# Kernel tuning notes

Measured on AMD Instinct MI355X. Metric: run time of the kernel, lower is better.

Reference implementation:

```python
import jax, jax.numpy as jnp
import numpy as np
from jax import lax

P_COARSE, P_FINE = 8, 4
EMBED_DIM = 128


def _patchify(x, p):
    # torch unfold(kernel=p, stride=p) then transpose: [B, Hp*Wp, C*p*p]
    B, C, H, W = x.shape
    Hp, Wp = H // p, W // p
    t = x.reshape(B, C, Hp, p, Wp, p).transpose(0, 2, 4, 1, 3, 5)
    return t.reshape(B, Hp * Wp, C * p * p), Hp, Wp


def _edge_map(x):
    gray = x.mean(axis=1, keepdims=True)
    kx = jnp.array([[-1., 0., 1.], [-2., 0., 2.], [-1., 0., 1.]], gray.dtype)[None, None]
    ky = jnp.array([[-1., -2., -1.], [0., 0., 0.], [1., 2., 1.]], gray.dtype)[None, None]
    pad = [(1, 1), (1, 1)]
    sx = lax.conv_general_dilated(gray, kx, (1, 1), pad)
    sy = lax.conv_general_dilated(gray, ky, (1, 1), pad)
    e = jnp.sqrt(sx * sx + sy * sy)
    B, _, H, W = e.shape
    # avg_pool2d(4, stride=4)
    return e.reshape(B, 1, H // 4, 4, W // 4, 4).mean(axis=(3, 5))


def _compact(tok, m):
    # stream-compact masked rows to the front, zero-pad the rest (pad_sequence semantics, padded to full Nf)
    Nf, D = tok.shape
    pos = jnp.cumsum(m) - 1
    pos = jnp.where(m, pos, Nf)  # unmasked rows go to overflow slot
    out = jnp.zeros((Nf + 1, D), tok.dtype).at[pos].set(tok)
    return out[:Nf]


def setup_inputs() -> dict:
    key = jax.random.key(0)
    ks = jax.random.split(key, 6)
    D = EMBED_DIM
    pd_c = 1 * P_COARSE * P_COARSE
    pd_f = 1 * P_FINE * P_FINE
    return {
        "x": jax.random.normal(ks[0], (8, 1, 512, 512), jnp.float32),
        "w_coarse": jax.random.normal(ks[1], (pd_c, D), jnp.float32) / np.sqrt(pd_c),
        "b_coarse": jnp.zeros((D,), jnp.float32),
        "w_fine": jax.random.normal(ks[2], (pd_f, D), jnp.float32) / np.sqrt(pd_f),
        "b_fine": jnp.zeros((D,), jnp.float32),
        "type_emb": jax.random.normal(ks[3], (2, D), jnp.float32) * 0.02,
    }


def reference(x, w_coarse, b_coarse, w_fine, b_fine, type_emb):
    B = x.shape[0]
    # coarse branch
    pc, Hc, Wc = _patchify(x, P_COARSE)
    coarse = pc @ w_coarse + b_coarse + type_emb[0]  # [B, Nc, D]
    # edge-driven mask
    edges = _edge_map(x)  # [B,1,He,We]
    mask = edges > edges.mean(axis=(2, 3), keepdims=True)
    # fine branch
    pf, Hf, Wf = _patchify(x, P_FINE)
    fine = pf @ w_fine + b_fine  # [B, Nf, D]
    # nearest upsample mask to (Hf, Wf): integer factor repeat
    m = mask[:, 0]
    m = jnp.repeat(jnp.repeat(m, Hf // m.shape[1], axis=1), Wf // m.shape[2], axis=2)
    mask_flat = m.reshape(B, -1)  # [B, Nf]
    fine_c = jax.vmap(_compact)(fine, mask_flat) + type_emb[1]
    tokens = jnp.concatenate([coarse, fine_c], axis=1)
    return tokens, mask_flat
```

## Files before the change

kernel.cpp:

```cpp
#include <hip/hip_runtime.h>

#define IMH 512
#define IMW 512
#define BATCH 8
#define NTOK 20480
#define NC 4096
#define NF 16384
#define ED 128

typedef float vf4 __attribute__((ext_vector_type(4)));

__device__ __forceinline__ void nt_store4(float* p, float a, float b, float c, float d) {
    vf4 v = {a, b, c, d};
    __builtin_nontemporal_store(v, (vf4*)p);
}
__device__ __forceinline__ void nt_store4v(float* p, float4 v) {
    nt_store4(p, v.x, v.y, v.z, v.w);
}

__global__ __launch_bounds__(256) void fused_edge_coarse(const float* __restrict__ x,
                                                         const float* __restrict__ wc,
                                                         const float* __restrict__ bc,
                                                         const float* __restrict__ temb,
                                                         float* __restrict__ out,
                                                         double* __restrict__ edges) {
    __shared__ float esm[66][68];
    int blk = blockIdx.x;
    int t = threadIdx.x;
    if (blk < 1024) {
        int b = blk >> 7;
        int pblk = (blk & 127) * 32;
        int wv = __builtin_amdgcn_readfirstlane(t >> 6);
        int lane = t & 63;
        int h = wv & 1;
        int p0 = pblk + (wv >> 1) * 16;
        int d = h * 64 + lane;
        float wcol[64];
        #pragma unroll
        for (int k = 0; k < 64; ++k) wcol[k] = wc[k * ED + d];
        float base = bc[d] + temb[d];
        const float* img = x + ((size_t)b * IMH + (p0 >> 6) * 8) * IMW + (p0 & 63) * 8;
        float* dst = out + ((size_t)b * NTOK + p0) * ED + d;
        #pragma unroll
        for (int p = 0; p < 16; ++p) {
            const float* pimg = img + p * 8;
            float acc = base;
            #pragma unroll
            for (int r = 0; r < 8; ++r) {
                const float* rp = pimg + r * IMW;
                acc += rp[0] * wcol[r * 8 + 0] + rp[1] * wcol[r * 8 + 1]
                     + rp[2] * wcol[r * 8 + 2] + rp[3] * wcol[r * 8 + 3]
                     + rp[4] * wcol[r * 8 + 4] + rp[5] * wcol[r * 8 + 5]
                     + rp[6] * wcol[r * 8 + 6] + rp[7] * wcol[r * 8 + 7];
            }
            __builtin_nontemporal_store(acc, dst + (size_t)p * ED);
        }
    } else {
        int blk2 = blk - 1024;
        int b = blk2 >> 6;
        int tile = blk2 & 63;
        int ty0 = (tile >> 3) * 64;
        int tx0 = (tile & 7) * 64;
        const float* img = x + (size_t)b * (IMH * IMW);
        for (int idx = t; idx < 66 * 66; idx += 256) {
            int r = idx / 66, c = idx - r * 66;
            int gy = ty0 - 1 + r, gx = tx0 - 1 + c;
            float v = 0.f;
            if (gy >= 0 && gy < IMH && gx >= 0 && gx < IMW) v = img[gy * IMW + gx];
            esm[r][c] = v;
        }
        __syncthreads();
        int cy = t >> 4, cx = t & 15;
        double acc = 0.0;
        #pragma unroll
        for (int dy = 0; dy < 4; ++dy) {
            int py = cy * 4 + dy + 1;
            #pragma unroll
            for (int dx = 0; dx < 4; ++dx) {
                int px = cx * 4 + dx + 1;
                double a00 = (double)esm[py - 1][px - 1];
                double a01 = (double)esm[py - 1][px];
                double a02 = (double)esm[py - 1][px + 1];
                double a10 = (double)esm[py][px - 1];
                double a12 = (double)esm[py][px + 1];
                double a20 = (double)esm[py + 1][px - 1];
                double a21 = (double)esm[py + 1][px];
                double a22 = (double)esm[py + 1][px + 1];
                double sx = (a02 + 2.0 * a12 + a22) - (a00 + 2.0 * a10 + a20);
                double sy = (a20 + 2.0 * a21 + a22) - (a00 + 2.0 * a01 + a02);
                acc += sqrt(sx * sx + sy * sy);
            }
        }
        int gy = (ty0 >> 2) + cy;
        int gx = (tx0 >> 2) + cx;
        edges[((size_t)b << 14) + gy * 128 + gx] = acc * (1.0 / 16.0);
    }
}

__global__ __launch_bounds__(1024) void scan_kernel(const double* __restrict__ edges,
                                                    int* __restrict__ pos,
                                                    int* __restrict__ Karr,
                                                    float* __restrict__ mask_out) {
    int b = blockIdx.x;
    const double* e = edges + ((size_t)b << 14);
    int t = threadIdx.x;
    int lane = t & 63, wid = t >> 6;
    double v[16];
    #pragma unroll
    for (int j = 0; j < 8; ++j) {
        double2 dv = *(const double2*)&e[t * 16 + j * 2];
        v[2 * j] = dv.x; v[2 * j + 1] = dv.y;
    }
    double s = 0.0;
    #pragma unroll
    for (int j = 0; j < 16; ++j) s += v[j];
    #pragma unroll
    for (int off = 32; off > 0; off >>= 1) s += __shfl_xor(s, off);
    __shared__ double wsum[16];
    __shared__ int wcnt[16];
    if (lane == 0) wsum[wid] = s;
    __syncthreads();
    double total = 0.0;
    #pragma unroll
    for (int w = 0; w < 16; ++w) total += wsum[w];
    double mean = total * (1.0 / 16384.0);
    int m[16], cnt = 0;
    #pragma unroll
    for (int j = 0; j < 16; ++j) { m[j] = (v[j] > mean) ? 1 : 0; cnt += m[j]; }
    int incl = cnt;
    #pragma unroll
    for (int off = 1; off < 64; off <<= 1) {
        int up = __shfl_up(incl, off);
        if (lane >= off) incl += up;
    }
    if (lane == 63) wcnt[wid] = incl;
    __syncthreads();
    int woff = 0, Ktot = 0;
    #pragma unroll
    for (int w = 0; w < 16; ++w) { int c = wcnt[w]; Ktot += c; if (w < wid) woff += c; }
    int run = woff + incl - cnt;
    float mf[16]; int pv[16];
    #pragma unroll
    for (int j = 0; j < 16; ++j) {
        pv[j] = m[j] ? run : -1;
        run += m[j];
        mf[j] = m[j] ? 1.0f : 0.0f;
    }
    float* mb = mask_out + ((size_t)b << 14) + t * 16;
    int* pb = pos + ((size_t)b << 14) + t * 16;
    #pragma unroll
    for (int q = 0; q < 4; ++q) {
        nt_store4(&mb[q * 4], mf[4 * q], mf[4 * q + 1], mf[4 * q + 2], mf[4 * q + 3]);
        *(int4*)&pb[q * 4] = make_int4(pv[4 * q], pv[4 * q + 1], pv[4 * q + 2], pv[4 * q + 3]);
    }
    if (t == 0) Karr[b] = Ktot;
}

__global__ __launch_bounds__(256) void fine_kernel(const float* __restrict__ x,
                                                   const float* __restrict__ wfp,
                                                   const float* __restrict__ bfp,
                                                   const float* __restrict__ temb,
                                                   const int* __restrict__ pos,
                                                   const int* __restrict__ Karr,
                                                   float* __restrict__ out) {
    int b = blockIdx.y;
    int i0 = blockIdx.x * 64;
    int hf = i0 >> 7;
    int wf0 = i0 & 127;
    int t = threadIdx.x;
    int d4 = t & 31;
    int g = t >> 5;
    __shared__ float smx[4][256];
    float4 wcol[16];
    #pragma unroll
    for (int k = 0; k < 16; ++k) wcol[k] = *(const float4*)&wfp[k * ED + d4 * 4];
    const float* img = x + ((size_t)b * IMH + hf * 4) * IMW + wf0 * 4;
    {
        int r = t >> 6, c4 = t & 63;
        *(float4*)&smx[r][c4 * 4] = *(const float4*)&img[r * IMW + c4 * 4];
    }
    __syncthreads();
    int K = Karr[b];
    const int* posb = pos + ((size_t)b << 14);
    float4 fill = *(const float4*)&temb[ED + d4 * 4];
    float4 bse = *(const float4*)&bfp[d4 * 4];
    float4 base = make_float4(bse.x + fill.x, bse.y + fill.y, bse.z + fill.z, bse.w + fill.w);
    float* tok = out + ((size_t)b * NTOK + NC) * ED;
    #pragma unroll
    for (int pp = 0; pp < 8; ++pp) {
        int p = g + pp * 8;
        int i = i0 + p;
        int ps = posb[i];
        if (ps >= 0) {
            float4 acc = base;
            #pragma unroll
            for (int r = 0; r < 4; ++r) {
                float4 vv = *(const float4*)&smx[r][p * 4];
                acc.x += vv.x * wcol[4 * r].x + vv.y * wcol[4 * r + 1].x + vv.z * wcol[4 * r + 2].x + vv.w * wcol[4 * r + 3].x;
                acc.y += vv.x * wcol[4 * r].y + vv.y * wcol[4 * r + 1].y + vv.z * wcol[4 * r + 2].y + vv.w * wcol[4 * r + 3].y;
                acc.z += vv.x * wcol[4 * r].z + vv.y * wcol[4 * r + 1].z + vv.z * wcol[4 * r + 2].z + vv.w * wcol[4 * r + 3].z;
                acc.w += vv.x * wcol[4 * r].w + vv.y * wcol[4 * r + 1].w + vv.z * wcol[4 * r + 2].w + vv.w * wcol[4 * r + 3].w;
            }
            nt_store4v(tok + ((size_t)ps * 32 + d4) * 4, acc);
        }
        if (i >= K) {
            nt_store4v(tok + ((size_t)i * 32 + d4) * 4, fill);
        }
    }
}

extern "C" void kernel_launch(void* const* d_in, const int* in_sizes, int n_in,
                              void* d_out, int out_size, void* d_ws, size_t ws_size,
                              hipStream_t stream) {
    const float* x    = (const float*)d_in[0];
    const float* wc   = (const float*)d_in[1];
    const float* bc   = (const float*)d_in[2];
    const float* wfp  = (const float*)d_in[3];
    const float* bfp  = (const float*)d_in[4];
    const float* temb = (const float*)d_in[5];
    float* out = (float*)d_out;

    double* edges = (double*)d_ws;
    int* pos  = (int*)((char*)d_ws + (size_t)BATCH * NF * sizeof(double));
    int* Karr = (int*)((char*)d_ws + (size_t)BATCH * NF * (sizeof(double) + sizeof(int)));

    float* mask_out = out + (size_t)BATCH * NTOK * ED;

    fused_edge_coarse<<<dim3(1536), 256, 0, stream>>>(x, wc, bc, temb, out, edges);
    scan_kernel<<<dim3(BATCH), 1024, 0, stream>>>(edges, pos, Karr, mask_out);
    fine_kernel<<<dim3(256, BATCH), 256, 0, stream>>>(x, wfp, bfp, temb, pos, Karr, out);
}
```

Baseline: 49.23 us.

## Fold scan into fine kernel using per-tile edge partial sums and bitmasks

Removes the separate single-block-per-batch scan kernel. The edge kernel now writes per-tile partial sums, and each fine block recomputes the batch mean, the mask bits and the prefix counts for its row from the edges buffer. Compaction positions come from popcount over 64-bit masks instead of a stored pos array. This saves one launch and a serialized 8-block kernel, at the cost of every fine block redundantly reading 128KB of edges per batch.

After: 51.22 us. +4.0%, slower.

```diff
diff --git a/kernel.cpp b/kernel.cpp
--- a/kernel.cpp
+++ b/kernel.cpp
@@ -18,20 +18,22 @@
     nt_store4(p, v.x, v.y, v.z, v.w);
 }
 
-__global__ __launch_bounds__(256) void fused_edge_coarse(const float* __restrict__ x,
-                                                         const float* __restrict__ wc,
-                                                         const float* __restrict__ bc,
-                                                         const float* __restrict__ temb,
-                                                         float* __restrict__ out,
-                                                         double* __restrict__ edges) {
+__global__ __launch_bounds__(256) void k1_edge_coarse(const float* __restrict__ x,
+                                                      const float* __restrict__ wc,
+                                                      const float* __restrict__ bc,
+                                                      const float* __restrict__ temb,
+                                                      float* __restrict__ out,
+                                                      double* __restrict__ edges,
+                                                      double* __restrict__ tsum) {
     __shared__ float esm[66][68];
+    __shared__ double dred[4];
     int blk = blockIdx.x;
     int t = threadIdx.x;
+    int lane = t & 63, wid = t >> 6;
     if (blk < 1024) {
         int b = blk >> 7;
         int pblk = (blk & 127) * 32;
         int wv = __builtin_amdgcn_readfirstlane(t >> 6);
-        int lane = t & 63;
         int h = wv & 1;
         int p0 = pblk + (wv >> 1) * 16;
         int d = h * 64 + lane;
@@ -91,108 +93,105 @@
                 acc += sqrt(sx * sx + sy * sy);
             }
         }
+        double cell = acc * (1.0 / 16.0);
         int gy = (ty0 >> 2) + cy;
         int gx = (tx0 >> 2) + cx;
-        edges[((size_t)b << 14) + gy * 128 + gx] = acc * (1.0 / 16.0);
-    }
-}
-
-__global__ __launch_bounds__(1024) void scan_kernel(const double* __restrict__ edges,
-                                                    int* __restrict__ pos,
-                                                    int* __restrict__ Karr,
-                                                    float* __restrict__ mask_out) {
-    int b = blockIdx.x;
-    const double* e = edges + ((size_t)b << 14);
+        edges[((size_t)b << 14) + gy * 128 + gx] = cell;
+        double sc = cell;
+        #pragma unroll
+        for (int off = 32; off > 0; off >>= 1) sc += __shfl_xor(sc, off);
+        if (lane == 0) dred[wid] = sc;
+        __syncthreads();
+        if (t == 0) tsum[b * 64 + tile] = dred[0] + dred[1] + dred[2] + dred[3];
+    }
+}
+
+__global__ __launch_bounds__(256) void k2_fine(const float* __restrict__ x,
+                                               const float* __restrict__ wfp,
+                                               const float* __restrict__ bfp,
+                                               const float* __restrict__ temb,
+                                               const double* __restrict__ edges,
+                                               const double* __restrict__ tsum,
+                                               float* __restrict__ out,
+                                               float* __restrict__ mask_out) {
+    int b = blockIdx.y;
+    int row = blockIdx.x;
     int t = threadIdx.x;
     int lane = t & 63, wid = t >> 6;
-    double v[16];
-    #pragma unroll
-    for (int j = 0; j < 8; ++j) {
-        double2 dv = *(const double2*)&e[t * 16 + j * 2];
-        v[2 * j] = dv.x; v[2 * j + 1] = dv.y;
-    }
-    double s = 0.0;
-    #pragma unroll
-    for (int j = 0; j < 16; ++j) s += v[j];
-    #pragma unroll
-    for (int off = 32; off > 0; off >>= 1) s += __shfl_xor(s, off);
-    __shared__ double wsum[16];
-    __shared__ int wcnt[16];
-    if (lane == 0) wsum[wid] = s;
-    __syncthreads();
+    __shared__ float smx[4][512];
+    __shared__ int excl_s[256];
+    __shared__ unsigned long long bits_s[256];
+    __shared__ int wtot[4];
+
+    const double* ts = tsum + b * 64;
     double total = 0.0;
     #pragma unroll
-    for (int w = 0; w < 16; ++w) total += wsum[w];
+    for (int j = 0; j < 64; ++j) total += ts[j];
     double mean = total * (1.0 / 16384.0);
-    int m[16], cnt = 0;
-    #pragma unroll
-    for (int j = 0; j < 16; ++j) { m[j] = (v[j] > mean) ? 1 : 0; cnt += m[j]; }
+
+    const double* e = edges + ((size_t)b << 14) + t * 64;
+    unsigned long long mybits = 0ULL;
+    #pragma unroll
+    for (int j = 0; j < 32; ++j) {
+        double2 dv = *(const double2*)&e[j * 2];
+        if (dv.x > mean) mybits |= (1ULL << (2 * j));
+        if (dv.y > mean) mybits |= (1ULL << (2 * j + 1));
+    }
+    int cnt = __popcll(mybits);
     int incl = cnt;
     #pragma unroll
     for (int off = 1; off < 64; off <<= 1) {
         int up = __shfl_up(incl, off);
         if (lane >= off) incl += up;
     }
-    if (lane == 63) wcnt[wid] = incl;
+    if (lane == 63) wtot[wid] = incl;
+    bits_s[t] = mybits;
     __syncthreads();
-    int woff = 0, Ktot = 0;
-    #pragma unroll
-    for (int w = 0; w < 16; ++w) { int c = wcnt[w]; Ktot += c; if (w < wid) woff += c; }
-    int run = woff + incl - cnt;
-    float mf[16]; int pv[16];
-    #pragma unroll
-    for (int j = 0; j < 16; ++j) {
-        pv[j] = m[j] ? run : -1;
-        run += m[j];
-        mf[j] = m[j] ? 1.0f : 0.0f;
-    }
-    float* mb = mask_out + ((size_t)b << 14) + t * 16;
-    int* pb = pos + ((size_t)b << 14) + t * 16;
-    #pragma unroll
-    for (int q = 0; q < 4; ++q) {
-        nt_store4(&mb[q * 4], mf[4 * q], mf[4 * q + 1], mf[4 * q + 2], mf[4 * q + 3]);
-        *(int4*)&pb[q * 4] = make_int4(pv[4 * q], pv[4 * q + 1], pv[4 * q + 2], pv[4 * q + 3]);
-    }
-    if (t == 0) Karr[b] = Ktot;
-}
-
-__global__ __launch_bounds__(256) void fine_kernel(const float* __restrict__ x,
-                                                   const float* __restrict__ wfp,
-                                                   const float* __restrict__ bfp,
-                                                   const float* __restrict__ temb,
-                                                   const int* __restrict__ pos,
-                                                   const int* __restrict__ Karr,
-                                                   float* __restrict__ out) {
-    int b = blockIdx.y;
-    int i0 = blockIdx.x * 64;
-    int hf = i0 >> 7;
-    int wf0 = i0 & 127;
-    int t = threadIdx.x;
+    int woff = 0, K = 0;
+    #pragma unroll
+    for (int w = 0; w < 4; ++w) { int c = wtot[w]; K += c; if (w < wid) woff += c; }
+    excl_s[t] = woff + incl - cnt;
+
+    const float* img = x + ((size_t)b * IMH + row * 4) * IMW;
+    #pragma unroll
+    for (int k = 0; k < 2; ++k) {
+        int idx = t + 256 * k;
+        int r = idx >> 7, c4 = idx & 127;
+        *(float4*)&smx[r][c4 * 4] = *(const float4*)&img[r * IMW + c4 * 4];
+    }
+    __syncthreads();
+
+    int base = excl_s[2 * row];
+    unsigned long long lo = bits_s[2 * row];
+    unsigned long long hi = bits_s[2 * row + 1];
+
+    if (t < 128) {
+        unsigned long long bb = (t < 64) ? lo : hi;
+        float mv = ((bb >> (t & 63)) & 1ULL) ? 1.0f : 0.0f;
+        __builtin_nontemporal_store(mv, mask_out + ((size_t)b << 14) + row * 128 + t);
+    }
+
     int d4 = t & 31;
     int g = t >> 5;
-    __shared__ float smx[4][256];
     float4 wcol[16];
     #pragma unroll
     for (int k = 0; k < 16; ++k) wcol[k] = *(const float4*)&wfp[k * ED + d4 * 4];
-    const float* img = x + ((size_t)b * IMH + hf * 4) * IMW + wf0 * 4;
-    {
-        int r = t >> 6, c4 = t & 63;
-        *(float4*)&smx[r][c4 * 4] = *(const float4*)&img[r * IMW + c4 * 4];
-    }
-    __syncthreads();
-    int K = Karr[b];
-    const int* posb = pos + ((size_t)b << 14);
     float4 fill = *(const float4*)&temb[ED + d4 * 4];
     float4 bse = *(const float4*)&bfp[d4 * 4];
-    float4 base = make_float4(bse.x + fill.x, bse.y + fill.y, bse.z + fill.z, bse.w + fill.w);
+    float4 fbase = make_float4(bse.x + fill.x, bse.y + fill.y, bse.z + fill.z, bse.w + fill.w);
     float* tok = out + ((size_t)b * NTOK + NC) * ED;
-    #pragma unroll
-    for (int pp = 0; pp < 8; ++pp) {
+    int i0 = row * 128;
+    #pragma unroll
+    for (int pp = 0; pp < 16; ++pp) {
         int p = g + pp * 8;
         int i = i0 + p;
-        int ps = posb[i];
-        if (ps >= 0) {
-            float4 acc = base;
+        unsigned long long bb = (p < 64) ? lo : hi;
+        if ((bb >> (p & 63)) & 1ULL) {
+            int below = (p < 64)
+                ? __popcll(lo & ((1ULL << p) - 1))
+                : __popcll(lo) + __popcll(hi & ((1ULL << (p - 64)) - 1));
+            int ps = base + below;
+            float4 acc = fbase;
             #pragma unroll
             for (int r = 0; r < 4; ++r) {
                 float4 vv = *(const float4*)&smx[r][p * 4];
@@ -220,13 +219,11 @@
     const float* temb = (const float*)d_in[5];
     float* out = (float*)d_out;
 
-    double* edges = (double*)d_ws;
-    int* pos  = (int*)((char*)d_ws + (size_t)BATCH * NF * sizeof(double));
-    int* Karr = (int*)((char*)d_ws + (size_t)BATCH * NF * (sizeof(double) + sizeof(int)));
-
+    char* wsb = (char*)d_ws;
+    double* edges = (double*)wsb;
+    double* tsum  = (double*)(wsb + (size_t)BATCH * NF * 8);
     float* mask_out = out + (size_t)BATCH * NTOK * ED;
 
-    fused_edge_coarse<<<dim3(1536), 256, 0, stream>>>(x, wc, bc, temb, out, edges);
-    scan_kernel<<<dim3(BATCH), 1024, 0, stream>>>(edges, pos, Karr, mask_out);
-    fine_kernel<<<dim3(256, BATCH), 256, 0, stream>>>(x, wfp, bfp, temb, pos, Karr, out);
-}
+    k1_edge_coarse<<<dim3(1536), 256, 0, stream>>>(x, wc, bc, temb, out, edges, tsum);
+    k2_fine<<<dim3(128, BATCH), 256, 0, stream>>>(x, wfp, bfp, temb, edges, tsum, out, mask_out);
+}
```

## Move coarse projection into fine kernel and precompute per-tile edge sums

Applied to the files above, without the earlier changes.

Splits the edge computation into its own kernel, which also emits per-tile partial sums so the scan no longer reduces the whole edge map itself. The coarse patch projection moves out of the first kernel into a combined coarse+fine kernel, where each block handles two fine tiles. Nontemporal stores are replaced with normal stores. This shortens the critical path ahead of the scan and removes a launch's worth of tail, but leaves the coarse work waiting on the serial scan instead of overlapping with it.

Result: slower. 54.68 us (+11.1%).

```diff
diff --git a/kernel.cpp b/kernel.cpp
--- a/kernel.cpp
+++ b/kernel.cpp
@@ -8,30 +8,133 @@
 #define NF 16384
 #define ED 128
 
-typedef float vf4 __attribute__((ext_vector_type(4)));
-
-__device__ __forceinline__ void nt_store4(float* p, float a, float b, float c, float d) {
-    vf4 v = {a, b, c, d};
-    __builtin_nontemporal_store(v, (vf4*)p);
-}
-__device__ __forceinline__ void nt_store4v(float* p, float4 v) {
-    nt_store4(p, v.x, v.y, v.z, v.w);
-}
-
-__global__ __launch_bounds__(256) void fused_edge_coarse(const float* __restrict__ x,
-                                                         const float* __restrict__ wc,
-                                                         const float* __restrict__ bc,
-                                                         const float* __restrict__ temb,
-                                                         float* __restrict__ out,
-                                                         double* __restrict__ edges) {
+__global__ __launch_bounds__(256) void k_edge(const float* __restrict__ x,
+                                              double* __restrict__ edges,
+                                              double* __restrict__ tsum) {
     __shared__ float esm[66][68];
+    __shared__ double dred[4];
     int blk = blockIdx.x;
     int t = threadIdx.x;
-    if (blk < 1024) {
-        int b = blk >> 7;
-        int pblk = (blk & 127) * 32;
+    int lane = t & 63, wid = t >> 6;
+    int b = blk >> 6;
+    int tile = blk & 63;
+    int ty0 = (tile >> 3) * 64;
+    int tx0 = (tile & 7) * 64;
+    const float* img = x + (size_t)b * (IMH * IMW);
+    for (int idx = t; idx < 66 * 66; idx += 256) {
+        int r = idx / 66, c = idx - r * 66;
+        int gy = ty0 - 1 + r, gx = tx0 - 1 + c;
+        float v = 0.f;
+        if (gy >= 0 && gy < IMH && gx >= 0 && gx < IMW) v = img[gy * IMW + gx];
+        esm[r][c] = v;
+    }
+    __syncthreads();
+    int cy = t >> 4, cx = t & 15;
+    double acc = 0.0;
+    #pragma unroll
+    for (int dy = 0; dy < 4; ++dy) {
+        int py = cy * 4 + dy + 1;
+        #pragma unroll
+        for (int dx = 0; dx < 4; ++dx) {
+            int px = cx * 4 + dx + 1;
+            double a00 = (double)esm[py - 1][px - 1];
+            double a01 = (double)esm[py - 1][px];
+            double a02 = (double)esm[py - 1][px + 1];
+            double a10 = (double)esm[py][px - 1];
+            double a12 = (double)esm[py][px + 1];
+            double a20 = (double)esm[py + 1][px - 1];
+            double a21 = (double)esm[py + 1][px];
+            double a22 = (double)esm[py + 1][px + 1];
+            double sx = (a02 + 2.0 * a12 + a22) - (a00 + 2.0 * a10 + a20);
+            double sy = (a20 + 2.0 * a21 + a22) - (a00 + 2.0 * a01 + a02);
+            acc += sqrt(sx * sx + sy * sy);
+        }
+    }
+    double cell = acc * (1.0 / 16.0);
+    int gy = (ty0 >> 2) + cy;
+    int gx = (tx0 >> 2) + cx;
+    edges[((size_t)b << 14) + gy * 128 + gx] = cell;
+    double sc = cell;
+    #pragma unroll
+    for (int off = 32; off > 0; off >>= 1) sc += __shfl_xor(sc, off);
+    if (lane == 0) dred[wid] = sc;
+    __syncthreads();
+    if (t == 0) tsum[b * 64 + tile] = dred[0] + dred[1] + dred[2] + dred[3];
+}
+
+__global__ __launch_bounds__(1024) void k_scan(const double* __restrict__ edges,
+                                               const double* __restrict__ tsum,
+                                               int* __restrict__ pos,
+                                               int* __restrict__ Karr,
+                                               float* __restrict__ mask_out) {
+    int b = blockIdx.x;
+    int t = threadIdx.x;
+    int lane = t & 63, wid = t >> 6;
+    __shared__ int wcnt[16];
+    const double* ts = tsum + b * 64;
+    double total = 0.0;
+    #pragma unroll
+    for (int j = 0; j < 64; ++j) total += ts[j];
+    double mean = total * (1.0 / 16384.0);
+
+    const double* e = edges + ((size_t)b << 14);
+    double v[16];
+    #pragma unroll
+    for (int j = 0; j < 8; ++j) {
+        double2 dv = *(const double2*)&e[t * 16 + j * 2];
+        v[2 * j] = dv.x; v[2 * j + 1] = dv.y;
+    }
+    int m[16], cnt = 0;
+    #pragma unroll
+    for (int j = 0; j < 16; ++j) { m[j] = (v[j] > mean) ? 1 : 0; cnt += m[j]; }
+    int incl = cnt;
+    #pragma unroll
+    for (int off = 1; off < 64; off <<= 1) {
+        int up = __shfl_up(incl, off);
+        if (lane >= off) incl += up;
+    }
+    if (lane == 63) wcnt[wid] = incl;
+    __syncthreads();
+    int woff = 0, Ktot = 0;
+    #pragma unroll
+    for (int w = 0; w < 16; ++w) { int c = wcnt[w]; Ktot += c; if (w < wid) woff += c; }
+    int run = woff + incl - cnt;
+    float mf[16]; int pv[16];
+    #pragma unroll
+    for (int j = 0; j < 16; ++j) {
+        pv[j] = m[j] ? run : -1;
+        run += m[j];
+        mf[j] = m[j] ? 1.0f : 0.0f;
+    }
+    float* mb = mask_out + ((size_t)b << 14) + t * 16;
+    int* pb = pos + ((size_t)b << 14) + t * 16;
+    #pragma unroll
+    for (int q = 0; q < 4; ++q) {
+        *(float4*)&mb[q * 4] = make_float4(mf[4 * q], mf[4 * q + 1], mf[4 * q + 2], mf[4 * q + 3]);
+        *(int4*)&pb[q * 4] = make_int4(pv[4 * q], pv[4 * q + 1], pv[4 * q + 2], pv[4 * q + 3]);
+    }
+    if (t == 0) Karr[b] = Ktot;
+}
+
+__global__ __launch_bounds__(256) void k_mega(const float* __restrict__ x,
+                                              const float* __restrict__ wc,
+                                              const float* __restrict__ bc,
+                                              const float* __restrict__ wfp,
+                                              const float* __restrict__ bfp,
+                                              const float* __restrict__ temb,
+                                              const int* __restrict__ pos,
+                                              const int* __restrict__ Karr,
+                                              float* __restrict__ out) {
+    __shared__ float smx[4][256];
+    int blk = blockIdx.x;
+    int t = threadIdx.x;
+    int lane = t & 63;
+    int b = blk >> 7;
+    int r128 = blk & 127;
+
+    {
+        int pblk = r128 * 32;
         int wv = __builtin_amdgcn_readfirstlane(t >> 6);
-        int lane = t & 63;
         int h = wv & 1;
         int p0 = pblk + (wv >> 1) * 16;
         int d = h * 64 + lane;
@@ -53,158 +156,55 @@
                      + rp[4] * wcol[r * 8 + 4] + rp[5] * wcol[r * 8 + 5]
                      + rp[6] * wcol[r * 8 + 6] + rp[7] * wcol[r * 8 + 7];
             }
-            __builtin_nontemporal_store(acc, dst + (size_t)p * ED);
-        }
-    } else {
-        int blk2 = blk - 1024;
-        int b = blk2 >> 6;
-        int tile = blk2 & 63;
-        int ty0 = (tile >> 3) * 64;
-        int tx0 = (tile & 7) * 64;
-        const float* img = x + (size_t)b * (IMH * IMW);
-        for (int idx = t; idx < 66 * 66; idx += 256) {
-            int r = idx / 66, c = idx - r * 66;
-            int gy = ty0 - 1 + r, gx = tx0 - 1 + c;
-            float v = 0.f;
-            if (gy >= 0 && gy < IMH && gx >= 0 && gx < IMW) v = img[gy * IMW + gx];
-            esm[r][c] = v;
-        }
-        __syncthreads();
-        int cy = t >> 4, cx = t & 15;
-        double acc = 0.0;
-        #pragma unroll
-        for (int dy = 0; dy < 4; ++dy) {
-            int py = cy * 4 + dy + 1;
-            #pragma unroll
-            for (int dx = 0; dx < 4; ++dx) {
-                int px = cx * 4 + dx + 1;
-                double a00 = (double)esm[py - 1][px - 1];
-                double a01 = (double)esm[py - 1][px];
-                double a02 = (double)esm[py - 1][px + 1];
-                double a10 = (double)esm[py][px - 1];
-                double a12 = (double)esm[py][px + 1];
-                double a20 = (double)esm[py + 1][px - 1];
-                double a21 = (double)esm[py + 1][px];
-                double a22 = (double)esm[py + 1][px + 1];
-                double sx = (a02 + 2.0 * a12 + a22) - (a00 + 2.0 * a10 + a20);
-                double sy = (a20 + 2.0 * a21 + a22) - (a00 + 2.0 * a01 + a02);
-                acc += sqrt(sx * sx + sy * sy);
-            }
-        }
-        int gy = (ty0 >> 2) + cy;
-        int gx = (tx0 >> 2) + cx;
-        edges[((size_t)b << 14) + gy * 128 + gx] = acc * (1.0 / 16.0);
-    }
-}
-
-__global__ __launch_bounds__(1024) void scan_kernel(const double* __restrict__ edges,
-                                                    int* __restrict__ pos,
-                                                    int* __restrict__ Karr,
-                                                    float* __restrict__ mask_out) {
-    int b = blockIdx.x;
-    const double* e = edges + ((size_t)b << 14);
-    int t = threadIdx.x;
-    int lane = t & 63, wid = t >> 6;
-    double v[16];
-    #pragma unroll
-    for (int j = 0; j < 8; ++j) {
-        double2 dv = *(const double2*)&e[t * 16 + j * 2];
-        v[2 * j] = dv.x; v[2 * j + 1] = dv.y;
-    }
-    double s = 0.0;
-    #pragma unroll
-    for (int j = 0; j < 16; ++j) s += v[j];
-    #pragma unroll
-    for (int off = 32; off > 0; off >>= 1) s += __shfl_xor(s, off);
-    __shared__ double wsum[16];
-    __shared__ int wcnt[16];
-    if (lane == 0) wsum[wid] = s;
-    __syncthreads();
-    double total = 0.0;
-    #pragma unroll
-    for (int w = 0; w < 16; ++w) total += wsum[w];
-    double mean = total * (1.0 / 16384.0);
-    int m[16], cnt = 0;
-    #pragma unroll
-    for (int j = 0; j < 16; ++j) { m[j] = (v[j] > mean) ? 1 : 0; cnt += m[j]; }
-    int incl = cnt;
-    #pragma unroll
-    for (int off = 1; off < 64; off <<= 1) {
-        int up = __shfl_up(incl, off);
-        if (lane >= off) incl += up;
-    }
-    if (lane == 63) wcnt[wid] = incl;
-    __syncthreads();
-    int woff = 0, Ktot = 0;
-    #pragma unroll
-    for (int w = 0; w < 16; ++w) { int c = wcnt[w]; Ktot += c; if (w < wid) woff += c; }
-    int run = woff + incl - cnt;
-    float mf[16]; int pv[16];
-    #pragma unroll
-    for (int j = 0; j < 16; ++j) {
-        pv[j] = m[j] ? run : -1;
-        run += m[j];
-        mf[j] = m[j] ? 1.0f : 0.0f;
-    }
-    float* mb = mask_out + ((size_t)b << 14) + t * 16;
-    int* pb = pos + ((size_t)b << 14) + t * 16;
-    #pragma unroll
-    for (int q = 0; q < 4; ++q) {
-        nt_store4(&mb[q * 4], mf[4 * q], mf[4 * q + 1], mf[4 * q + 2], mf[4 * q + 3]);
-        *(int4*)&pb[q * 4] = make_int4(pv[4 * q], pv[4 * q + 1], pv[4 * q + 2], pv[4 * q + 3]);
-    }
-    if (t == 0) Karr[b] = Ktot;
-}
-
-__global__ __launch_bounds__(256) void fine_kernel(const float* __restrict__ x,
-                                                   const float* __restrict__ wfp,
-                                                   const float* __restrict__ bfp,
-                                                   const float* __restrict__ temb,
-                                                   const int* __restrict__ pos,
-                                                   const int* __restrict__ Karr,
-                                                   float* __restrict__ out) {
-    int b = blockIdx.y;
-    int i0 = blockIdx.x * 64;
-    int hf = i0 >> 7;
-    int wf0 = i0 & 127;
-    int t = threadIdx.x;
+            dst[(size_t)p * ED] = acc;
+        }
+    }
+    asm volatile("" ::: "memory");
+
     int d4 = t & 31;
     int g = t >> 5;
-    __shared__ float smx[4][256];
     float4 wcol[16];
     #pragma unroll
     for (int k = 0; k < 16; ++k) wcol[k] = *(const float4*)&wfp[k * ED + d4 * 4];
-    const float* img = x + ((size_t)b * IMH + hf * 4) * IMW + wf0 * 4;
-    {
-        int r = t >> 6, c4 = t & 63;
-        *(float4*)&smx[r][c4 * 4] = *(const float4*)&img[r * IMW + c4 * 4];
-    }
-    __syncthreads();
+    float4 fill = *(const float4*)&temb[ED + d4 * 4];
+    float4 bse = *(const float4*)&bfp[d4 * 4];
+    float4 fbase = make_float4(bse.x + fill.x, bse.y + fill.y, bse.z + fill.z, bse.w + fill.w);
     int K = Karr[b];
     const int* posb = pos + ((size_t)b << 14);
-    float4 fill = *(const float4*)&temb[ED + d4 * 4];
-    float4 bse = *(const float4*)&bfp[d4 * 4];
-    float4 base = make_float4(bse.x + fill.x, bse.y + fill.y, bse.z + fill.z, bse.w + fill.w);
     float* tok = out + ((size_t)b * NTOK + NC) * ED;
-    #pragma unroll
-    for (int pp = 0; pp < 8; ++pp) {
-        int p = g + pp * 8;
-        int i = i0 + p;
-        int ps = posb[i];
-        if (ps >= 0) {
-            float4 acc = base;
-            #pragma unroll
-            for (int r = 0; r < 4; ++r) {
-                float4 vv = *(const float4*)&smx[r][p * 4];
-                acc.x += vv.x * wcol[4 * r].x + vv.y * wcol[4 * r + 1].x + vv.z * wcol[4 * r + 2].x + vv.w * wcol[4 * r + 3].x;
-                acc.y += vv.x * wcol[4 * r].y + vv.y * wcol[4 * r + 1].y + vv.z * wcol[4 * r + 2].y + vv.w * wcol[4 * r + 3].y;
-                acc.z += vv.x * wcol[4 * r].z + vv.y * wcol[4 * r + 1].z + vv.z * wcol[4 * r + 2].z + vv.w * wcol[4 * r + 3].z;
-                acc.w += vv.x * wcol[4 * r].w + vv.y * wcol[4 * r + 1].w + vv.z * wcol[4 * r + 2].w + vv.w * wcol[4 * r + 3].w;
+
+    #pragma unroll
+    for (int u = 0; u < 2; ++u) {
+        int i0 = (r128 * 2 + u) * 64;
+        int hf = i0 >> 7;
+        int wf0 = i0 & 127;
+        const float* img = x + ((size_t)b * IMH + hf * 4) * IMW + wf0 * 4;
+        __syncthreads();
+        {
+            int r = t >> 6, c4 = t & 63;
+            *(float4*)&smx[r][c4 * 4] = *(const float4*)&img[r * IMW + c4 * 4];
+        }
+        __syncthreads();
+        #pragma unroll
+        for (int pp = 0; pp < 8; ++pp) {
+            int p = g + pp * 8;
+            int i = i0 + p;
+            int ps = posb[i];
+            if (ps >= 0) {
+                float4 acc = fbase;
+                #pragma unroll
+                for (int r = 0; r < 4; ++r) {
+                    float4 vv = *(const float4*)&smx[r][p * 4];
+                    acc.x += vv.x * wcol[4 * r].x + vv.y * wcol[4 * r + 1].x + vv.z * wcol[4 * r + 2].x + vv.w * wcol[4 * r + 3].x;
+                    acc.y += vv.x * wcol[4 * r].y + vv.y * wcol[4 * r + 1].y + vv.z * wcol[4 * r + 2].y + vv.w * wcol[4 * r + 3].y;
+                    acc.z += vv.x * wcol[4 * r].z + vv.y * wcol[4 * r + 1].z + vv.z * wcol[4 * r + 2].z + vv.w * wcol[4 * r + 3].z;
+                    acc.w += vv.x * wcol[4 * r].w + vv.y * wcol[4 * r + 1].w + vv.z * wcol[4 * r + 2].w + vv.w * wcol[4 * r + 3].w;
+                }
+                *(float4*)(tok + ((size_t)ps * 32 + d4) * 4) = acc;
             }
-            nt_store4v(tok + ((size_t)ps * 32 + d4) * 4, acc);
-        }
-        if (i >= K) {
-            nt_store4v(tok + ((size_t)i * 32 + d4) * 4, fill);
+            if (i >= K) {
+                *(float4*)(tok + ((size_t)i * 32 + d4) * 4) = fill;
+            }
         }
     }
 }
@@ -220,13 +220,14 @@
     const float* temb = (const float*)d_in[5];
     float* out = (float*)d_out;
 
-    double* edges = (double*)d_ws;
-    int* pos  = (int*)((char*)d_ws + (size_t)BATCH * NF * sizeof(double));
-    int* Karr = (int*)((char*)d_ws + (size_t)BATCH * NF * (sizeof(double) + sizeof(int)));
-
+    char* wsb = (char*)d_ws;
+    double* edges = (double*)wsb;
+    double* tsum  = (double*)(wsb + (size_t)BATCH * NF * 8);
+    int* pos  = (int*)(wsb + (size_t)BATCH * NF * 8 + 4096);
+    int* Karr = (int*)(wsb + (size_t)BATCH * NF * 8 + 4096 + (size_t)BATCH * NF * 4);
     float* mask_out = out + (size_t)BATCH * NTOK * ED;
 
-    fused_edge_coarse<<<dim3(1536), 256, 0, stream>>>(x, wc, bc, temb, out, edges);
-    scan_kernel<<<dim3(BATCH), 1024, 0, stream>>>(edges, pos, Karr, mask_out);
-    fine_kernel<<<dim3(256, BATCH), 256, 0, stream>>>(x, wfp, bfp, temb, pos, Karr, out);
-}
+    k_edge<<<dim3(512), 256, 0, stream>>>(x, edges, tsum);
+    k_scan<<<dim3(BATCH), 1024, 0, stream>>>(edges, tsum, pos, Karr, mask_out);
+    k_mega<<<dim3(1024), 256, 0, stream>>>(x, wc, bc, wfp, bfp, temb, pos, Karr, out);
+}
```
